# Kernel tuning notes

Hardware: AMD Instinct MI355X
Metric: run time of the kernel (lower is better)

Reference implementation:

```python
import jax, jax.numpy as jnp
import numpy as np

B = 256        # trees per batch
DEPTH = 10     # complete binary tree depth -> 2^10 - 1 = 1023 internal nodes
N = 2**DEPTH - 1
IN = 128       # input_size
H = 128        # hidden_size
C = 5          # num_classes


def setup_inputs() -> dict:
    key = jax.random.key(0)
    ks = jax.random.split(key, 13)
    gdim = IN + 2 * H  # concat(x, h_left, h_right)
    inp = {"x": jax.random.normal(ks[0], (B, N, IN), jnp.float32)}
    names = ["i", "fl", "fr", "o", "u"]
    for j, nm in enumerate(names):
        inp[f"W_{nm}"] = 0.05 * jax.random.normal(ks[1 + 2 * j], (H, gdim), jnp.float32)
        inp[f"b_{nm}"] = 0.05 * jax.random.normal(ks[2 + 2 * j], (H,), jnp.float32)
    inp["W_cls"] = 0.05 * jax.random.normal(ks[11], (C, H), jnp.float32)
    inp["b_cls"] = 0.05 * jax.random.normal(ks[12], (C,), jnp.float32)
    return inp


def reference(x, W_i, b_i, W_fl, b_fl, W_fr, b_fr, W_o, b_o, W_u, b_u, W_cls, b_cls):
    # Level-order complete binary tree: node k has children 2k+1, 2k+2.
    # Bottom-up sweep; below the deepest internal level all children are
    # empty nodes with h = c = 0 (matches the original base case).
    Bb = x.shape[0]
    h = jnp.zeros((Bb, 2 ** DEPTH, H), x.dtype)
    c = jnp.zeros_like(h)
    for d in range(DEPTH - 1, -1, -1):  # fixed, small structural loop
        n = 2 ** d
        start = n - 1  # level-order offset of level d
        xs = x[:, start:start + n]            # [B, n, IN]
        hl, hr = h[:, 0::2], h[:, 1::2]       # children of node j are 2j, 2j+1 (level-local)
        cl, cr = c[:, 0::2], c[:, 1::2]
        comb = jnp.concatenate([xs, hl, hr], axis=-1)  # [B, n, IN+2H]
        lin = lambda W, b: jnp.einsum('bng,og->bno', comb, W) + b
        i = jax.nn.sigmoid(lin(W_i, b_i))
        fl = jax.nn.sigmoid(lin(W_fl, b_fl))
        fr = jax.nn.sigmoid(lin(W_fr, b_fr))
        o = jax.nn.sigmoid(lin(W_o, b_o))
        u = jnp.tanh(lin(W_u, b_u))
        c = i * u + fl * cl + fr * cr
        h = o * jnp.tanh(c)
    root_h = h[:, 0]                          # [B, H]
    logits = root_h @ W_cls.T + b_cls         # [B, C]
    return logits
```

## Files before the change

### kernel.cpp

```cpp
#include <hip/hip_runtime.h>
#include <hip/hip_bf16.h>
#include <stdint.h>


#define BATCH 256
#define NTOT 1023
#define HDIM 128
#define NCLS 5
#define GDIM 384

typedef __bf16 bf16x8 __attribute__((ext_vector_type(8)));
typedef float f32x4 __attribute__((ext_vector_type(4)));

__device__ __forceinline__ float sigmoid_f(float v) { return 1.f / (1.f + __expf(-v)); }
__device__ __forceinline__ float tanh_f(float v) { return 1.f - 2.f / (1.f + __expf(2.f * v)); }

__device__ __forceinline__ void load_lds16(const void* g, void* l) {
  __builtin_amdgcn_global_load_lds((const __attribute__((address_space(1))) unsigned int*)g,
                                   (__attribute__((address_space(3))) unsigned int*)l, 16, 0, 0);
}

__global__ __launch_bounds__(256) void pack_w(
    const float* __restrict__ W0, const float* __restrict__ W1, const float* __restrict__ W2,
    const float* __restrict__ W3, const float* __restrict__ W4, __bf16* __restrict__ PW)
{
  int t = blockIdx.x * 256 + threadIdx.x;
  int lane = t & 63;
  int chunk = t >> 6;
  int ks = chunk % 12;
  int jf = (chunk / 12) & 7;
  int g = chunk / 96;
  const float* W = (g == 0) ? W0 : (g == 1) ? W1 : (g == 2) ? W2 : (g == 3) ? W3 : W4;
  const float* s = W + (size_t)(jf * 16 + (lane & 15)) * GDIM + ks * 32 + (lane >> 4) * 8;
  float4 v0 = *(const float4*)s;
  float4 v1 = *(const float4*)(s + 4);
  bf16x8 w;
  w[0] = (__bf16)v0.x; w[1] = (__bf16)v0.y; w[2] = (__bf16)v0.z; w[3] = (__bf16)v0.w;
  w[4] = (__bf16)v1.x; w[5] = (__bf16)v1.y; w[6] = (__bf16)v1.z; w[7] = (__bf16)v1.w;
  *(bf16x8*)(PW + (size_t)t * 8) = w;
}

template<bool LEAF>
__device__ __forceinline__ void tile_body(
    const float* __restrict__ x, const __bf16* __restrict__ PW,
    const __bf16* __restrict__ h_prev, const float* __restrict__ c_prev,
    __bf16* __restrict__ h_out, float* __restrict__ c_out,
    const float* __restrict__ bv0, const float* __restrict__ bv1,
    const float* __restrict__ bv2, const float* __restrict__ bv3,
    const float* __restrict__ bv4,
    int d, int m0, int j0, unsigned char* lds)
{
  const int tid = threadIdx.x;
  const int w = tid >> 6;
  const int l = tid & 63;
  const int l15 = l & 15;
  const int quad = l >> 4;
  const int q8 = quad * 8;
  const int mh = w & 1, jh = w >> 1;
  const int n = 1 << d;
  const int jfb = j0 >> 4;
  constexpr int NKT = LEAF ? 4 : 12;
  constexpr int NBC = LEAF ? 3 : 5;
  constexpr int NACC = LEAF ? 3 : 5;
  constexpr int BUFS = LEAF ? 16384 : 24576;
  constexpr int AI_O = LEAF ? 1 : 3;
  constexpr int AI_U = LEAF ? 2 : 4;

  const int ms = m0 + w * 16 + l15;
  const int bs = ms >> d;
  const int ids = ms & (n - 1);
  const float* xrow = x + ((size_t)bs * NTOT + (n - 1) + ids) * HDIM;
  const __bf16* hrow = LEAF ? (const __bf16*)nullptr
                            : h_prev + ((size_t)bs * 2 * n + 2 * ids) * HDIM;

  float cpl[2][2][4], cpr[2][2][4];
  if constexpr (!LEAF) {
#pragma unroll
    for (int jfl = 0; jfl < 2; ++jfl) {
      const int je = j0 + jh * 32 + jfl * 16 + l15;
#pragma unroll
      for (int mf = 0; mf < 2; ++mf) {
#pragma unroll
        for (int r = 0; r < 4; ++r) {
          const int me = m0 + mh * 32 + mf * 16 + quad * 4 + r;
          const int bb_ = me >> d;
          const int id = me & (n - 1);
          const size_t cbase = ((size_t)bb_ * 2 * n + 2 * id) * HDIM + je;
          cpl[jfl][mf][r] = c_prev[cbase];
          cpr[jfl][mf][r] = c_prev[cbase + HDIM];
        }
      }
    }
  }

  auto stage = [&](int ks) {
    unsigned char* Ab = lds + (ks & 1) * BUFS;
    unsigned char* Bb = Ab + 4096;
#pragma unroll
    for (int q = 0; q < NBC; ++q) {
      int c = w * NBC + q;
      int g;
      if (LEAF) { const int gm[3] = {0, 3, 4}; g = gm[c >> 2]; }
      else g = c >> 2;
      int jfl = c & 3;
      const __bf16* s = PW + (((size_t)(g * 8 + jfb + jfl) * 12 + ks) * 64 + l) * 8;
      load_lds16(s, Bb + c * 1024);
    }
    if (LEAF || ks < 4) {
      const float* s = xrow + ks * 32 + q8;
      float4 v0 = *(const float4*)s;
      float4 v1 = *(const float4*)(s + 4);
      bf16x8 wv;
      wv[0] = (__bf16)v0.x; wv[1] = (__bf16)v0.y; wv[2] = (__bf16)v0.z; wv[3] = (__bf16)v0.w;
      wv[4] = (__bf16)v1.x; wv[5] = (__bf16)v1.y; wv[6] = (__bf16)v1.z; wv[7] = (__bf16)v1.w;
      *(bf16x8*)(Ab + w * 1024 + l * 16) = wv;
    } else {
      int off = (ks < 8) ? (ks - 4) * 32 : 128 + (ks - 8) * 32;
      load_lds16(hrow + off + q8, Ab + w * 1024);
    }
  };

  f32x4 acc[2][2][NACC];
#pragma unroll
  for (int mf = 0; mf < 2; ++mf)
#pragma unroll
    for (int jfl = 0; jfl < 2; ++jfl)
#pragma unroll
      for (int ai = 0; ai < NACC; ++ai)
        acc[mf][jfl][ai] = (f32x4){0.f, 0.f, 0.f, 0.f};

  stage(0);
  for (int ks = 0; ks < NKT; ++ks) {
    __syncthreads();
    if (ks + 1 < NKT) stage(ks + 1);
    const unsigned char* Ab = lds + (ks & 1) * BUFS;
    const unsigned char* Bb = Ab + 4096;
    bf16x8 a0 = *(const bf16x8*)(Ab + (mh * 2 + 0) * 1024 + l * 16);
    bf16x8 a1 = *(const bf16x8*)(Ab + (mh * 2 + 1) * 1024 + l * 16);
#pragma unroll
    for (int ai = 0; ai < NACC; ++ai) {
#pragma unroll
      for (int jfl = 0; jfl < 2; ++jfl) {
        bf16x8 bb = *(const bf16x8*)(Bb + (ai * 4 + jh * 2 + jfl) * 1024 + l * 16);
        acc[0][jfl][ai] = __builtin_amdgcn_mfma_f32_16x16x32_bf16(a0, bb, acc[0][jfl][ai], 0, 0, 0);
        acc[1][jfl][ai] = __builtin_amdgcn_mfma_f32_16x16x32_bf16(a1, bb, acc[1][jfl][ai], 0, 0, 0);
      }
    }
  }

#pragma unroll
  for (int jfl = 0; jfl < 2; ++jfl) {
    const int je = j0 + jh * 32 + jfl * 16 + l15;
    const float b0 = bv0[je], b3 = bv3[je], b4 = bv4[je];
#pragma unroll
    for (int mf = 0; mf < 2; ++mf) {
#pragma unroll
      for (int r = 0; r < 4; ++r) {
        int me = m0 + mh * 32 + mf * 16 + quad * 4 + r;
        int b = me >> d;
        int id = me & (n - 1);
        float gi = sigmoid_f(acc[mf][jfl][0][r] + b0);
        float go = sigmoid_f(acc[mf][jfl][AI_O][r] + b3);
        float gu = tanh_f(acc[mf][jfl][AI_U][r] + b4);
        float cv = gi * gu;
        if constexpr (!LEAF) {
          float gl = sigmoid_f(acc[mf][jfl][1][r] + bv1[je]);
          float gr = sigmoid_f(acc[mf][jfl][2][r] + bv2[je]);
          cv += gl * cpl[jfl][mf][r] + gr * cpr[jfl][mf][r];
        }
        size_t ob = ((size_t)b * n + id) * HDIM + je;
        c_out[ob] = cv;
        h_out[ob] = (__bf16)(go * tanh_f(cv));
      }
    }
  }
}

template<bool LEAF>
__global__ __launch_bounds__(256, (LEAF ? 4 : 3)) void level_kernel(
    const float* __restrict__ x, const __bf16* __restrict__ PW,
    const float* __restrict__ bv0, const float* __restrict__ bv1,
    const float* __restrict__ bv2, const float* __restrict__ bv3,
    const float* __restrict__ bv4,
    const __bf16* __restrict__ h_prev, const float* __restrict__ c_prev,
    __bf16* __restrict__ h_out, float* __restrict__ c_out, int d)
{
  __shared__ unsigned char lds[LEAF ? 32768 : 49152];
  tile_body<LEAF>(x, PW, h_prev, c_prev, h_out, c_out,
                  bv0, bv1, bv2, bv3, bv4, d,
                  (int)blockIdx.x * 64, (int)blockIdx.y * 64, lds);
}

#define TB_P  81920
#define TB_Q  132096
#define CSTR  132

__global__ __launch_bounds__(256, 1) void tail_kernel(
    const float* __restrict__ x, const __bf16* __restrict__ PW,
    const float* __restrict__ bv0, const float* __restrict__ bv1,
    const float* __restrict__ bv2, const float* __restrict__ bv3,
    const float* __restrict__ bv4,
    const float* __restrict__ Wcls, const float* __restrict__ bcls,
    const __bf16* __restrict__ h6, const float* __restrict__ c6,
    float* __restrict__ out)
{
  __shared__ unsigned char lds[157184];
  const int b = blockIdx.x;
  const int tid = threadIdx.x;
  const int w = tid >> 6;
  const int l = tid & 63;
  const int l15 = l & 15;
  const int quad = l >> 4;
  const int q8 = quad * 8;

  unsigned char* Ph = lds + TB_P;
  float* Pc = (float*)(lds + TB_P + 16384);
  unsigned char* Qh = lds + TB_Q;
  float* Qc = (float*)(lds + TB_Q + 8192);

  {
    const __bf16* hs = h6 + (size_t)b * 64 * HDIM;
#pragma unroll
    for (int it = 0; it < 4; ++it) {
      int idx = it * 256 + tid;
      int node = idx >> 4, i8 = idx & 15;
      bf16x8 v = *(const bf16x8*)(hs + node * HDIM + i8 * 8);
      *(bf16x8*)(Ph + node * 256 + ((i8 * 16) ^ ((node & 7) << 4))) = v;
    }
    const float* cs = c6 + (size_t)b * 64 * HDIM;
#pragma unroll
    for (int it = 0; it < 8; ++it) {
      int idx = it * 256 + tid;
      int node = idx >> 5, seg = idx & 31;
      float4 v = *(const float4*)(cs + node * HDIM + seg * 4);
      *(float4*)(Pc + node * CSTR + seg * 4) = v;
    }
  }

  for (int d = 5; d >= 0; --d) {
    const int s = 5 - d;
    const int n = 1 << d;
    const int nmf = (d == 5) ? 2 : 1;
    unsigned char* prev_h = (s & 1) ? Qh : Ph;
    float*         prev_c = (s & 1) ? Qc : Pc;
    unsigned char* cur_h  = (s & 1) ? Ph : Qh;
    float*         cur_c  = (s & 1) ? Pc : Qc;

    bf16x8 xf[2][4];
#pragma unroll
    for (int mf = 0; mf < 2; ++mf) {
      const float* xr = x + ((size_t)b * NTOT + (n - 1) + mf * 16 + l15) * HDIM + q8;
#pragma unroll
      for (int ks = 0; ks < 4; ++ks) {
        float4 v0 = *(const float4*)(xr + ks * 32);
        float4 v1 = *(const float4*)(xr + ks * 32 + 4);
        bf16x8 t;
        t[0] = (__bf16)v0.x; t[1] = (__bf16)v0.y; t[2] = (__bf16)v0.z; t[3] = (__bf16)v0.w;
        t[4] = (__bf16)v1.x; t[5] = (__bf16)v1.y; t[6] = (__bf16)v1.z; t[7] = (__bf16)v1.w;
        xf[mf][ks] = t;
      }
    }

    auto stageB = [&](int ks) {
      unsigned char* Bb = lds + (ks & 1) * 40960;
#pragma unroll
      for (int q = 0; q < 10; ++q) {
        int c = w * 10 + q;
        const __bf16* src = PW + ((size_t)(c * 12 + ks) * 64 + l) * 8;
        load_lds16(src, Bb + c * 1024);
      }
    };

    f32x4 acc[2][2][5];
#pragma unroll
    for (int mf = 0; mf < 2; ++mf)
#pragma unroll
      for (int jfl = 0; jfl < 2; ++jfl)
#pragma unroll
        for (int g = 0; g < 5; ++g)
          acc[mf][jfl][g] = (f32x4){0.f, 0.f, 0.f, 0.f};

    stageB(0);
    for (int ks = 0; ks < 12; ++ks) {
      __syncthreads();
      if (ks < 11) stageB(ks + 1);
      const unsigned char* Bb = lds + (ks & 1) * 40960;
      bf16x8 a0, a1;
      if (ks < 4) {
        a0 = xf[0][ks];
        a1 = xf[1][ks];
      } else {
        const int o = (ks < 8) ? 0 : 1;
        const int col2 = (((ks - (o ? 8 : 4)) * 32) + q8) * 2;
        int n0 = 2 * l15 + o;
        int n1 = 2 * (16 + l15) + o;
        a0 = *(const bf16x8*)(prev_h + n0 * 256 + (col2 ^ ((n0 & 7) << 4)));
        a1 = *(const bf16x8*)(prev_h + n1 * 256 + (col2 ^ ((n1 & 7) << 4)));
      }
#pragma unroll
      for (int g = 0; g < 5; ++g) {
#pragma unroll
        for (int jfl = 0; jfl < 2; ++jfl) {
          bf16x8 bb = *(const bf16x8*)(Bb + (g * 8 + w * 2 + jfl) * 1024 + l * 16);
          acc[0][jfl][g] = __builtin_amdgcn_mfma_f32_16x16x32_bf16(a0, bb, acc[0][jfl][g], 0, 0, 0);
          if (nmf == 2)
            acc[1][jfl][g] = __builtin_amdgcn_mfma_f32_16x16x32_bf16(a1, bb, acc[1][jfl][g], 0, 0, 0);
        }
      }
    }

#pragma unroll
    for (int jfl = 0; jfl < 2; ++jfl) {
      const int je = w * 32 + jfl * 16 + l15;
      const float b0 = bv0[je], b1 = bv1[je], b2 = bv2[je], b3 = bv3[je], b4 = bv4[je];
#pragma unroll
      for (int mf = 0; mf < 2; ++mf) {
#pragma unroll
        for (int r = 0; r < 4; ++r) {
          const int me = mf * 16 + quad * 4 + r;
          if (me < n) {
            float gi = sigmoid_f(acc[mf][jfl][0][r] + b0);
            float gl = sigmoid_f(acc[mf][jfl][1][r] + b1);
            float gr = sigmoid_f(acc[mf][jfl][2][r] + b2);
            float go = sigmoid_f(acc[mf][jfl][3][r] + b3);
            float gu = tanh_f(acc[mf][jfl][4][r] + b4);
            float cv = gi * gu + gl * prev_c[(2 * me) * CSTR + je]
                               + gr * prev_c[(2 * me + 1) * CSTR + je];
            cur_c[me * CSTR + je] = cv;
            *(__bf16*)(cur_h + me * 256 + ((je * 2) ^ ((me & 7) << 4))) =
                (__bf16)(go * tanh_f(cv));
          }
        }
      }
    }
  }

  __syncthreads();
  if (tid < NCLS) {
    float sacc = bcls[tid];
    for (int k = 0; k < HDIM; ++k)
      sacc += (float)(*(const __bf16*)(Ph + k * 2)) * Wcls[tid * HDIM + k];
    out[(size_t)b * NCLS + tid] = sacc;
  }
}

extern "C" void kernel_launch(void* const* d_in, const int* in_sizes, int n_in,
                              void* d_out, int out_size, void* d_ws, size_t ws_size,
                              hipStream_t stream) {
  const float* x  = (const float*)d_in[0];
  const float* W[5]  = {(const float*)d_in[1], (const float*)d_in[3], (const float*)d_in[5],
                        (const float*)d_in[7], (const float*)d_in[9]};
  const float* bv[5] = {(const float*)d_in[2], (const float*)d_in[4], (const float*)d_in[6],
                        (const float*)d_in[8], (const float*)d_in[10]};
  const float* Wcls = (const float*)d_in[11];
  const float* bcls = (const float*)d_in[12];

  uint8_t* ws = (uint8_t*)d_ws;
  __bf16* hb0 = (__bf16*)ws;
  __bf16* hb1 = (__bf16*)(ws + 33554432);
  float*  cb0 = (float*)(ws + 50331648);
  float*  cb1 = (float*)(ws + 117440512);
  __bf16* PW  = (__bf16*)(ws + 150994944);

  pack_w<<<120, 256, 0, stream>>>(W[0], W[1], W[2], W[3], W[4], PW);

  level_kernel<true><<<dim3(2048, 2), 256, 0, stream>>>(
      x, PW, bv[0], bv[1], bv[2], bv[3], bv[4], hb1, cb1, hb0, cb0, 9);
  for (int d = 8; d >= 6; --d) {
    const int p = 9 - d;
    __bf16* h_out = (p & 1) ? hb1 : hb0;
    float*  c_out = (p & 1) ? cb1 : cb0;
    const __bf16* h_prev = (p & 1) ? hb0 : hb1;
    const float*  c_prev = (p & 1) ? cb0 : cb1;
    dim3 grid((BATCH << d) >> 6, 2);
    level_kernel<false><<<grid, 256, 0, stream>>>(
        x, PW, bv[0], bv[1], bv[2], bv[3], bv[4], h_prev, c_prev, h_out, c_out, d);
  }
  tail_kernel<<<BATCH, 256, 0, stream>>>(
      x, PW, bv[0], bv[1], bv[2], bv[3], bv[4],
      Wcls, bcls, hb1, cb1, (float*)d_out);
}
```

Measured before the change: 463.5 us.

## Double M tile to 128 rows with 512-thread blocks sharing weight tiles

Level kernels now use 512-thread blocks covering 128 node rows per block instead of 64. Each staged weight chunk in LDS is therefore reused by twice as many rows, which halves the weight traffic per node. Weight-chunk staging is redistributed across 8 waves, and the LDS layout is resized to fit the larger A tile. The early register prefetch of child c values is dropped in favour of loading them in the epilogue, which frees registers for occupancy but exposes global load latency at the end of the tile.

Measured after the change: 468.3 us. Within noise of the previous version (+1.0%).

```diff
diff --git a/kernel.cpp b/kernel.cpp
--- a/kernel.cpp
+++ b/kernel.cpp
@@ -56,13 +56,15 @@
   const int l15 = l & 15;
   const int quad = l >> 4;
   const int q8 = quad * 8;
-  const int mh = w & 1, jh = w >> 1;
+  const int mh = w >> 1;
+  const int jh = w & 1;
   const int n = 1 << d;
   const int jfb = j0 >> 4;
   constexpr int NKT = LEAF ? 4 : 12;
-  constexpr int NBC = LEAF ? 3 : 5;
   constexpr int NACC = LEAF ? 3 : 5;
-  constexpr int BUFS = LEAF ? 16384 : 24576;
+  constexpr int NCH = 4 * NACC;
+  constexpr int NBC = LEAF ? 2 : 3;
+  constexpr int BUFS = 8192 + NCH * 1024;
   constexpr int AI_O = LEAF ? 1 : 3;
   constexpr int AI_U = LEAF ? 2 : 4;
 
@@ -73,38 +75,18 @@
   const __bf16* hrow = LEAF ? (const __bf16*)nullptr
                             : h_prev + ((size_t)bs * 2 * n + 2 * ids) * HDIM;
 
-  float cpl[2][2][4], cpr[2][2][4];
-  if constexpr (!LEAF) {
-#pragma unroll
-    for (int jfl = 0; jfl < 2; ++jfl) {
-      const int je = j0 + jh * 32 + jfl * 16 + l15;
-#pragma unroll
-      for (int mf = 0; mf < 2; ++mf) {
-#pragma unroll
-        for (int r = 0; r < 4; ++r) {
-          const int me = m0 + mh * 32 + mf * 16 + quad * 4 + r;
-          const int bb_ = me >> d;
-          const int id = me & (n - 1);
-          const size_t cbase = ((size_t)bb_ * 2 * n + 2 * id) * HDIM + je;
-          cpl[jfl][mf][r] = c_prev[cbase];
-          cpr[jfl][mf][r] = c_prev[cbase + HDIM];
-        }
-      }
-    }
-  }
-
   auto stage = [&](int ks) {
     unsigned char* Ab = lds + (ks & 1) * BUFS;
-    unsigned char* Bb = Ab + 4096;
+    unsigned char* Bb = Ab + 8192;
 #pragma unroll
     for (int q = 0; q < NBC; ++q) {
-      int c = w * NBC + q;
-      int g;
-      if (LEAF) { const int gm[3] = {0, 3, 4}; g = gm[c >> 2]; }
-      else g = c >> 2;
-      int jfl = c & 3;
-      const __bf16* s = PW + (((size_t)(g * 8 + jfb + jfl) * 12 + ks) * 64 + l) * 8;
-      load_lds16(s, Bb + c * 1024);
+      int c = w + q * 8;
+      if (c < NCH) {
+        int ai = c >> 2, jfl = c & 3;
+        int g = LEAF ? (ai ? ai + 2 : 0) : ai;
+        const __bf16* s = PW + (((size_t)(g * 8 + jfb + jfl) * 12 + ks) * 64 + l) * 8;
+        load_lds16(s, Bb + c * 1024);
+      }
     }
     if (LEAF || ks < 4) {
       const float* s = xrow + ks * 32 + q8;
@@ -134,7 +116,7 @@
     __syncthreads();
     if (ks + 1 < NKT) stage(ks + 1);
     const unsigned char* Ab = lds + (ks & 1) * BUFS;
-    const unsigned char* Bb = Ab + 4096;
+    const unsigned char* Bb = Ab + 8192;
     bf16x8 a0 = *(const bf16x8*)(Ab + (mh * 2 + 0) * 1024 + l * 16);
     bf16x8 a1 = *(const bf16x8*)(Ab + (mh * 2 + 1) * 1024 + l * 16);
 #pragma unroll
@@ -166,7 +148,8 @@
         if constexpr (!LEAF) {
           float gl = sigmoid_f(acc[mf][jfl][1][r] + bv1[je]);
           float gr = sigmoid_f(acc[mf][jfl][2][r] + bv2[je]);
-          cv += gl * cpl[jfl][mf][r] + gr * cpr[jfl][mf][r];
+          size_t cbase = ((size_t)b * 2 * n + 2 * id) * HDIM + je;
+          cv += gl * c_prev[cbase] + gr * c_prev[cbase + HDIM];
         }
         size_t ob = ((size_t)b * n + id) * HDIM + je;
         c_out[ob] = cv;
@@ -177,7 +160,7 @@
 }
 
 template<bool LEAF>
-__global__ __launch_bounds__(256, (LEAF ? 4 : 3)) void level_kernel(
+__global__ __launch_bounds__(512, 2) void level_kernel(
     const float* __restrict__ x, const __bf16* __restrict__ PW,
     const float* __restrict__ bv0, const float* __restrict__ bv1,
     const float* __restrict__ bv2, const float* __restrict__ bv3,
@@ -185,10 +168,10 @@
     const __bf16* __restrict__ h_prev, const float* __restrict__ c_prev,
     __bf16* __restrict__ h_out, float* __restrict__ c_out, int d)
 {
-  __shared__ unsigned char lds[LEAF ? 32768 : 49152];
+  __shared__ unsigned char lds[LEAF ? 40960 : 57344];
   tile_body<LEAF>(x, PW, h_prev, c_prev, h_out, c_out,
                   bv0, bv1, bv2, bv3, bv4, d,
-                  (int)blockIdx.x * 64, (int)blockIdx.y * 64, lds);
+                  (int)blockIdx.x * 128, (int)blockIdx.y * 64, lds);
 }
 
 #define TB_P  81920
@@ -364,7 +347,7 @@
 
   pack_w<<<120, 256, 0, stream>>>(W[0], W[1], W[2], W[3], W[4], PW);
 
-  level_kernel<true><<<dim3(2048, 2), 256, 0, stream>>>(
+  level_kernel<true><<<dim3((BATCH << 9) >> 7, 2), 512, 0, stream>>>(
       x, PW, bv[0], bv[1], bv[2], bv[3], bv[4], hb1, cb1, hb0, cb0, 9);
   for (int d = 8; d >= 6; --d) {
     const int p = 9 - d;
@@ -372,8 +355,8 @@
     float*  c_out = (p & 1) ? cb1 : cb0;
     const __bf16* h_prev = (p & 1) ? hb0 : hb1;
     const float*  c_prev = (p & 1) ? cb0 : cb1;
-    dim3 grid((BATCH << d) >> 6, 2);
-    level_kernel<false><<<grid, 256, 0, stream>>>(
+    dim3 grid((BATCH << d) >> 7, 2);
+    level_kernel<false><<<grid, 512, 0, stream>>>(
         x, PW, bv[0], bv[1], bv[2], bv[3], bv[4], h_prev, c_prev, h_out, c_out, d);
   }
   tail_kernel<<<BATCH, 256, 0, stream>>>(
```
